# Optimization experiments

Hardware: AMD Instinct MI355X
Metric: run time of the kernel (lower is better)

Reference implementation:

```python
import math
import jax, jax.numpy as jnp
import numpy as np

B, T, E, NH = 2, 4096, 768, 12
HS = E // NH

def setup_inputs() -> dict:
    key = jax.random.key(0)
    k1, k2, k3 = jax.random.split(key, 3)
    x = jax.random.normal(k1, (B, T, E), dtype=jnp.float32)
    W_attn = jax.random.normal(k2, (E, 3 * E), dtype=jnp.float32) * (1.0 / math.sqrt(E))
    b_attn = jnp.zeros((3 * E,), dtype=jnp.float32)
    W_proj = jax.random.normal(k3, (E, E), dtype=jnp.float32) * (1.0 / math.sqrt(E))
    b_proj = jnp.zeros((E,), dtype=jnp.float32)
    return {"x": x, "W_attn": W_attn, "b_attn": b_attn, "W_proj": W_proj, "b_proj": b_proj}

def reference(x, W_attn, b_attn, W_proj, b_proj):
    b, t, e = x.shape
    nh, hs = NH, e // NH
    # QKV projection; split order matches einops '(a nh hs)' with a=3 outermost
    qkv = x @ W_attn + b_attn                      # [b, t, 3e]
    qkv = qkv.reshape(b, t, 3, nh, hs)
    q, k, v = jnp.moveaxis(qkv, 2, 0)              # each [b, t, nh, hs]
    q = jnp.transpose(q, (0, 2, 1, 3))             # [b, nh, t, hs]
    k = jnp.transpose(k, (0, 2, 1, 3))
    v = jnp.transpose(v, (0, 2, 1, 3))
    attn = jnp.einsum('bnth,bnsh->bnts', q, k) * (1.0 / math.sqrt(hs))  # [b, nh, t, t]
    causal = jnp.tril(jnp.ones((t, t), dtype=bool))
    attn = jnp.where(causal[None, None], attn, jnp.float32(-jnp.inf))
    attn = jax.nn.softmax(attn, axis=-1)
    y = jnp.einsum('bnts,bnsh->bnth', attn, v)     # [b, nh, t, hs]
    y = jnp.transpose(y, (0, 2, 1, 3)).reshape(b, t, e)
    return y @ W_proj + b_proj
```

## Files before the change

### kernel.cpp

```cpp
#include <hip/hip_runtime.h>
#include <hip/hip_bf16.h>
#include <cmath>

#define B_   2
#define T_   4096
#define E_   768
#define NH_  12
#define HS_  64
#define QKV_ROW (3 * E_)
#define LSE_N (B_ * NH_ * T_)
#define BTE   (B_ * T_ * E_)

typedef __attribute__((ext_vector_type(8))) short bf16x8;
typedef __attribute__((ext_vector_type(4))) float f32x4;

__device__ __forceinline__ unsigned short f2bf(float f) {
    __hip_bfloat16 h = __float2bfloat16(f);
    return __builtin_bit_cast(unsigned short, h);
}
__device__ __forceinline__ float bf2f(unsigned short s) {
    unsigned int u = (unsigned int)s << 16;
    return __builtin_bit_cast(float, u);
}

#define GLOAD16(gptr, lptr)                                             \
    __builtin_amdgcn_global_load_lds(                                   \
        (const __attribute__((address_space(1))) void*)(gptr),          \
        (__attribute__((address_space(3))) void*)(lptr), 16, 0, 0)

__global__ __launch_bounds__(256) void cvt_x_kernel(
    const float* __restrict__ x, unsigned short* __restrict__ xb)
{
    const int i = (blockIdx.x * 256 + threadIdx.x) * 8;
    const float4 v0 = *(const float4*)&x[i];
    const float4 v1 = *(const float4*)&x[i + 4];
    unsigned short o[8];
    o[0] = f2bf(v0.x); o[1] = f2bf(v0.y); o[2] = f2bf(v0.z); o[3] = f2bf(v0.w);
    o[4] = f2bf(v1.x); o[5] = f2bf(v1.y); o[6] = f2bf(v1.z); o[7] = f2bf(v1.w);
    *(int4*)&xb[i] = *(const int4*)o;
}

__global__ __launch_bounds__(256) void transpose_w_kernel(
    const float* __restrict__ W, unsigned short* __restrict__ Wt, int K, int N)
{
    __shared__ float tile[64][65];
    const int k0  = blockIdx.y * 64;
    const int n0  = blockIdx.x * 64;
    const int tid = threadIdx.x;
    const int tc  = tid & 15;
    const int tr  = tid >> 4;
#pragma unroll
    for (int i = 0; i < 4; ++i) {
        const int k = tr + i * 16;
        const float4 v = *(const float4*)&W[(size_t)(k0 + k) * N + n0 + tc * 4];
        tile[k][tc * 4 + 0] = v.x; tile[k][tc * 4 + 1] = v.y;
        tile[k][tc * 4 + 2] = v.z; tile[k][tc * 4 + 3] = v.w;
    }
    __syncthreads();
    const int nr = tid >> 2;
    const int kc = (tid & 3) * 16;
    unsigned short o[16];
#pragma unroll
    for (int j = 0; j < 16; ++j) o[j] = f2bf(tile[kc + j][nr]);
    unsigned short* dst = &Wt[(size_t)(n0 + nr) * K + k0 + kc];
    *(int4*)dst       = *(const int4*)&o[0];
    *(int4*)(dst + 8) = *(const int4*)&o[8];
}

template<bool OUT_BF16, bool QSCALE>
__global__ __launch_bounds__(256) void gemm_bt_kernel(
    const unsigned short* __restrict__ A,
    const unsigned short* __restrict__ Bt,
    const float* __restrict__ bias, void* __restrict__ Cout,
    int M, int N, int K, int lda)
{
    __shared__ __align__(16) unsigned short Als[128 * 64];
    __shared__ __align__(16) unsigned short Bls[128 * 64];

    const int tid  = threadIdx.x;
    const int m0   = blockIdx.y * 128;
    const int n0   = blockIdx.x * 128;
    const int w    = tid >> 6;
    const int lane = tid & 63;
    const int lr   = lane & 15;
    const int lk   = lane >> 4;
    const int wm   = (w >> 1) * 64;
    const int wn   = (w & 1) * 64;

    f32x4 acc[4][4];
#pragma unroll
    for (int i = 0; i < 4; ++i)
#pragma unroll
        for (int j = 0; j < 4; ++j) acc[i][j] = (f32x4){0.f, 0.f, 0.f, 0.f};

    for (int k0 = 0; k0 < K; k0 += 64) {
        __syncthreads();
#pragma unroll
        for (int c = 0; c < 4; ++c) {
            const int idx = c * 256 + tid;
            const int row = idx >> 3;
            const int g   = (tid & 7) ^ (row & 7);
            GLOAD16(&A[(size_t)(m0 + row) * lda + k0 + g * 8], &Als[idx * 8]);
        }
#pragma unroll
        for (int c = 0; c < 4; ++c) {
            const int idx = c * 256 + tid;
            const int row = idx >> 3;
            const int g   = (tid & 7) ^ (row & 7);
            GLOAD16(&Bt[(size_t)(n0 + row) * K + k0 + g * 8], &Bls[idx * 8]);
        }
        __syncthreads();

#pragma unroll
        for (int kk = 0; kk < 2; ++kk) {
            bf16x8 a[4], b[4];
            const int gp = ((kk * 4 + lk) ^ (lr & 7)) << 3;
#pragma unroll
            for (int i = 0; i < 4; ++i) {
                a[i] = *(const bf16x8*)&Als[(wm + i * 16 + lr) * 64 + gp];
                b[i] = *(const bf16x8*)&Bls[(wn + i * 16 + lr) * 64 + gp];
            }
#pragma unroll
            for (int i = 0; i < 4; ++i)
#pragma unroll
                for (int j = 0; j < 4; ++j)
                    acc[i][j] = __builtin_amdgcn_mfma_f32_16x16x32_bf16(
                        b[j], a[i], acc[i][j], 0, 0, 0);
        }
    }

    const float beta = 0.18033688011f;
#pragma unroll
    for (int i = 0; i < 4; ++i) {
        const int row = m0 + wm + i * 16 + lr;
#pragma unroll
        for (int j = 0; j < 4; ++j) {
            const int nbase = n0 + wn + j * 16 + lk * 4;
            const float4 bv = *(const float4*)&bias[nbase];
            float v0 = acc[i][j][0] + bv.x;
            float v1 = acc[i][j][1] + bv.y;
            float v2 = acc[i][j][2] + bv.z;
            float v3 = acc[i][j][3] + bv.w;
            if (QSCALE && nbase < E_) {
                v0 *= beta; v1 *= beta; v2 *= beta; v3 *= beta;
            }
            if (OUT_BF16) {
                ushort4 o;
                o.x = f2bf(v0); o.y = f2bf(v1); o.z = f2bf(v2); o.w = f2bf(v3);
                *(ushort4*)&((unsigned short*)Cout)[(size_t)row * N + nbase] = o;
            } else {
                float4 o; o.x = v0; o.y = v1; o.z = v2; o.w = v3;
                *(float4*)&((float*)Cout)[(size_t)row * N + nbase] = o;
            }
        }
    }
}

__global__ __launch_bounds__(256) void flash_kernel(
    const unsigned short* __restrict__ qkv,
    unsigned short* __restrict__ y_part,
    float* __restrict__ lsum)
{
    __shared__ __align__(16) unsigned short K_lds[64][72];
    __shared__ __align__(16) unsigned short Vt[64][72];

    const int tid  = threadIdx.x;
    const int w    = tid >> 6;
    const int lane = tid & 63;
    const int lr   = lane & 15;
    const int lk   = lane >> 4;

    const int bid  = blockIdx.x;
    const int xcd  = bid & 7;
    const int rr   = bid >> 3;
    const int g    = (rr >> 5) * 8 + xcd;
    const int head = g >> 1;
    const int z    = g & 1;
    const int qb_lo = rr & 31;
    const int b    = head / NH_;
    const int nh   = head % NH_;
    const int qb_hi = 63 - qb_lo;
    const int q0_lo = qb_lo * 64;
    const int q0_hi = qb_hi * 64;

    const unsigned short* qkv_b = qkv + (size_t)b * T_ * QKV_ROW;

    bf16x8 qf_lo[2], qf_hi[2];
    {
        const unsigned short* qrl =
            qkv_b + (size_t)(q0_lo + w * 16 + lr) * QKV_ROW + nh * HS_;
        qf_lo[0] = *(const bf16x8*)(qrl + lk * 8);
        qf_lo[1] = *(const bf16x8*)(qrl + 32 + lk * 8);
        const unsigned short* qrh =
            qkv_b + (size_t)(q0_hi + w * 16 + lr) * QKV_ROW + nh * HS_;
        qf_hi[0] = *(const bf16x8*)(qrh + lk * 8);
        qf_hi[1] = *(const bf16x8*)(qrh + 32 + lk * 8);
    }

    bf16x8 af1;
    {
        const short one = (lr == 0) ? (short)0x3F80 : (short)0;
#pragma unroll
        for (int j = 0; j < 8; ++j) af1[j] = one;
    }

    f32x4 acc_lo[4], acc_hi[4];
    f32x4 accl_lo = (f32x4){0.f, 0.f, 0.f, 0.f};
    f32x4 accl_hi = (f32x4){0.f, 0.f, 0.f, 0.f};
#pragma unroll
    for (int i = 0; i < 4; ++i) {
        acc_lo[i] = (f32x4){0.f, 0.f, 0.f, 0.f};
        acc_hi[i] = (f32x4){0.f, 0.f, 0.f, 0.f};
    }

    const int sr = tid >> 2;
    const int sc = (tid & 3) * 16;

    auto softmax_pack = [&](f32x4* st, int q0, int kv0, bool diag,
                            bf16x8& pf0, bf16x8& pf1) {
        const int tq = q0 + w * 16 + lr;
        if (diag) {
#pragma unroll
            for (int cb = 0; cb < 4; ++cb)
#pragma unroll
                for (int r = 0; r < 4; ++r) {
                    const int tk = kv0 + cb * 16 + lk * 4 + r;
                    if (tk > tq) st[cb][r] = -INFINITY;
                }
        }
#pragma unroll
        for (int r = 0; r < 4; ++r) {
            pf0[r]     = (short)f2bf(exp2f(st[0][r]));
            pf0[r + 4] = (short)f2bf(exp2f(st[1][r]));
            pf1[r]     = (short)f2bf(exp2f(st[2][r]));
            pf1[r + 4] = (short)f2bf(exp2f(st[3][r]));
        }
    };

    int4 k01r, k23r, v01r, v23r;
    auto load_regs = [&](int j) {
        const unsigned short* krow =
            qkv_b + (size_t)(j * 64 + sr) * QKV_ROW + E_ + nh * HS_ + sc;
        const unsigned short* vrow = krow + E_;
        k01r = *(const int4*)krow;
        k23r = *(const int4*)(krow + 8);
        v01r = *(const int4*)vrow;
        v23r = *(const int4*)(vrow + 8);
    };

    load_regs(z);
    for (int j = z; j <= qb_hi; ) {
        const int kv0 = j * 64;
        const bool do_lo = (j <= qb_lo);
        __syncthreads();
        {
            *(int4*)&K_lds[sr][sc]     = k01r;
            *(int4*)&K_lds[sr][sc + 8] = k23r;
            const unsigned short* vs0 = (const unsigned short*)&v01r;
            const unsigned short* vs1 = (const unsigned short*)&v23r;
            const int kvhi = sr >> 3, kvlo = sr & 7;
#pragma unroll
            for (int i = 0; i < 8; ++i) {
                const int h = sc + i;
                Vt[h][((kvhi ^ (h >> 3)) << 3) + kvlo] = vs0[i];
            }
#pragma unroll
            for (int i = 0; i < 8; ++i) {
                const int h = sc + 8 + i;
                Vt[h][((kvhi ^ (h >> 3)) << 3) + kvlo] = vs1[i];
            }
        }
        __syncthreads();

        const int jn = j + 2;
        if (jn <= qb_hi) load_regs(jn);

        bf16x8 kf[4][2];
#pragma unroll
        for (int cb = 0; cb < 4; ++cb)
#pragma unroll
            for (int ks = 0; ks < 2; ++ks)
                kf[cb][ks] = *(const bf16x8*)&K_lds[cb * 16 + lr][ks * 32 + lk * 8];

        bf16x8 vf[4][2];
#pragma unroll
        for (int cb2 = 0; cb2 < 4; ++cb2) {
            const int row = cb2 * 16 + lr;
            const int sw  = row >> 3;
#pragma unroll
            for (int ks = 0; ks < 2; ++ks) {
                const int cA = ((4 * ks + (lk >> 1)) ^ sw);
                const int cB = ((4 * ks + 2 + (lk >> 1)) ^ sw);
                const int off = 4 * (lk & 1);
                ushort4 a = *(const ushort4*)&Vt[row][cA * 8 + off];
                ushort4 bq = *(const ushort4*)&Vt[row][cB * 8 + off];
                bf16x8 v;
                v[0] = (short)a.x;  v[1] = (short)a.y;
                v[2] = (short)a.z;  v[3] = (short)a.w;
                v[4] = (short)bq.x; v[5] = (short)bq.y;
                v[6] = (short)bq.z; v[7] = (short)bq.w;
                vf[cb2][ks] = v;
            }
        }

        f32x4 st_hi[4], st_lo[4];
        __builtin_amdgcn_s_setprio(1);
#pragma unroll
        for (int cb = 0; cb < 4; ++cb) {
            st_hi[cb] = (f32x4){0.f, 0.f, 0.f, 0.f};
            st_hi[cb] = __builtin_amdgcn_mfma_f32_16x16x32_bf16(kf[cb][0], qf_hi[0], st_hi[cb], 0, 0, 0);
            st_hi[cb] = __builtin_amdgcn_mfma_f32_16x16x32_bf16(kf[cb][1], qf_hi[1], st_hi[cb], 0, 0, 0);
        }
        if (do_lo) {
#pragma unroll
            for (int cb = 0; cb < 4; ++cb) {
                st_lo[cb] = (f32x4){0.f, 0.f, 0.f, 0.f};
                st_lo[cb] = __builtin_amdgcn_mfma_f32_16x16x32_bf16(kf[cb][0], qf_lo[0], st_lo[cb], 0, 0, 0);
                st_lo[cb] = __builtin_amdgcn_mfma_f32_16x16x32_bf16(kf[cb][1], qf_lo[1], st_lo[cb], 0, 0, 0);
            }
        }
        __builtin_amdgcn_s_setprio(0);

        bf16x8 pf0, pf1;
        softmax_pack(st_hi, q0_hi, kv0, j == qb_hi, pf0, pf1);
        __builtin_amdgcn_s_setprio(1);
#pragma unroll
        for (int cb2 = 0; cb2 < 4; ++cb2) {
            acc_hi[cb2] = __builtin_amdgcn_mfma_f32_16x16x32_bf16(vf[cb2][0], pf0, acc_hi[cb2], 0, 0, 0);
            acc_hi[cb2] = __builtin_amdgcn_mfma_f32_16x16x32_bf16(vf[cb2][1], pf1, acc_hi[cb2], 0, 0, 0);
        }
        accl_hi = __builtin_amdgcn_mfma_f32_16x16x32_bf16(af1, pf0, accl_hi, 0, 0, 0);
        accl_hi = __builtin_amdgcn_mfma_f32_16x16x32_bf16(af1, pf1, accl_hi, 0, 0, 0);
        __builtin_amdgcn_s_setprio(0);

        if (do_lo) {
            softmax_pack(st_lo, q0_lo, kv0, j == qb_lo, pf0, pf1);
            __builtin_amdgcn_s_setprio(1);
#pragma unroll
            for (int cb2 = 0; cb2 < 4; ++cb2) {
                acc_lo[cb2] = __builtin_amdgcn_mfma_f32_16x16x32_bf16(vf[cb2][0], pf0, acc_lo[cb2], 0, 0, 0);
                acc_lo[cb2] = __builtin_amdgcn_mfma_f32_16x16x32_bf16(vf[cb2][1], pf1, acc_lo[cb2], 0, 0, 0);
            }
            accl_lo = __builtin_amdgcn_mfma_f32_16x16x32_bf16(af1, pf0, accl_lo, 0, 0, 0);
            accl_lo = __builtin_amdgcn_mfma_f32_16x16x32_bf16(af1, pf1, accl_lo, 0, 0, 0);
            __builtin_amdgcn_s_setprio(0);
        }
        j = jn;
    }

    {
        const float lh = __shfl(accl_hi[0], lr);
        const float ll = __shfl(accl_lo[0], lr);
        unsigned short* yp = y_part + (size_t)z * BTE;
        const float li_hi = (lh > 0.f) ? 1.0f / lh : 0.f;
        const float li_lo = (ll > 0.f) ? 1.0f / ll : 0.f;
        const int tq_hi = q0_hi + w * 16 + lr;
        const int tq_lo = q0_lo + w * 16 + lr;
        unsigned short* yh = &yp[(size_t)(b * T_ + tq_hi) * E_ + nh * HS_];
        unsigned short* yl = &yp[(size_t)(b * T_ + tq_lo) * E_ + nh * HS_];
#pragma unroll
        for (int cb2 = 0; cb2 < 4; ++cb2) {
            ushort4 oh, ol;
            oh.x = f2bf(acc_hi[cb2][0] * li_hi); oh.y = f2bf(acc_hi[cb2][1] * li_hi);
            oh.z = f2bf(acc_hi[cb2][2] * li_hi); oh.w = f2bf(acc_hi[cb2][3] * li_hi);
            ol.x = f2bf(acc_lo[cb2][0] * li_lo); ol.y = f2bf(acc_lo[cb2][1] * li_lo);
            ol.z = f2bf(acc_lo[cb2][2] * li_lo); ol.w = f2bf(acc_lo[cb2][3] * li_lo);
            *(ushort4*)&yh[cb2 * 16 + lk * 4] = oh;
            *(ushort4*)&yl[cb2 * 16 + lk * 4] = ol;
        }
        if (lk == 0) {
            float* lz = lsum + (size_t)z * LSE_N + (size_t)head * T_;
            lz[tq_hi] = lh;
            lz[tq_lo] = ll;
        }
    }
}

__global__ __launch_bounds__(256) void merge_kernel(
    const unsigned short* __restrict__ y_part,
    const float* __restrict__ lsum,
    unsigned short* __restrict__ qkv)
{
    const int i  = blockIdx.x * 256 + threadIdx.x;
    const int e0 = i * 8;
    const int row = e0 / E_;
    const int e   = e0 - row * E_;
    const int nh  = e >> 6;
    const int lidx = ((row >> 12) * NH_ + nh) * T_ + (row & (T_ - 1));
    const float l0 = lsum[lidx];
    const float l1 = lsum[LSE_N + lidx];
    const float inv = 1.0f / (l0 + l1);
    const float w0 = l0 * inv, w1 = l1 * inv;
    bf16x8 p0 = *(const bf16x8*)&y_part[e0];
    bf16x8 p1 = *(const bf16x8*)&y_part[(size_t)BTE + e0];
    ushort4 oa, ob;
    unsigned short o[8];
#pragma unroll
    for (int jj = 0; jj < 8; ++jj)
        o[jj] = f2bf(w0 * bf2f((unsigned short)p0[jj]) +
                     w1 * bf2f((unsigned short)p1[jj]));
    oa.x = o[0]; oa.y = o[1]; oa.z = o[2]; oa.w = o[3];
    ob.x = o[4]; ob.y = o[5]; ob.z = o[6]; ob.w = o[7];
    unsigned short* dst = &qkv[(size_t)row * QKV_ROW + e];
    *(ushort4*)dst = oa;
    *(ushort4*)(dst + 4) = ob;
}

extern "C" void kernel_launch(void* const* d_in, const int* in_sizes, int n_in,
                              void* d_out, int out_size, void* d_ws, size_t ws_size,
                              hipStream_t stream)
{
    const float* x      = (const float*)d_in[0];
    const float* W_attn = (const float*)d_in[1];
    const float* b_attn = (const float*)d_in[2];
    const float* W_proj = (const float*)d_in[3];
    const float* b_proj = (const float*)d_in[4];
    float* out = (float*)d_out;

    char* ws = (char*)d_ws;
    unsigned short* qkv_ws  = (unsigned short*)ws;
    float*          lsum_ws = (float*)(ws + 37748736);
    unsigned short* x_bf16  = (unsigned short*)(ws + 38535168);
    unsigned short* wt_attn = (unsigned short*)(ws + 51118080);
    unsigned short* wt_proj = (unsigned short*)(ws + 54657024);
    unsigned short* y_part  = (unsigned short*)d_out;

    dim3 blk(256);

    cvt_x_kernel<<<dim3(BTE / 8 / 256), blk, 0, stream>>>(x, x_bf16);
    transpose_w_kernel<<<dim3(QKV_ROW / 64, E_ / 64), blk, 0, stream>>>(W_attn, wt_attn, E_, QKV_ROW);
    transpose_w_kernel<<<dim3(E_ / 64, E_ / 64), blk, 0, stream>>>(W_proj, wt_proj, E_, E_);

    gemm_bt_kernel<true, true><<<dim3(QKV_ROW / 128, (B_ * T_) / 128), blk, 0, stream>>>(
        x_bf16, wt_attn, b_attn, (void*)qkv_ws, B_ * T_, QKV_ROW, E_, E_);

    flash_kernel<<<dim3((T_ / 128) * B_ * NH_ * 2), blk, 0, stream>>>(qkv_ws, y_part, lsum_ws);

    merge_kernel<<<dim3(BTE / 8 / 256), blk, 0, stream>>>(y_part, lsum_ws, qkv_ws);

    gemm_bt_kernel<false, false><<<dim3(E_ / 128, (B_ * T_) / 128), blk, 0, stream>>>(
        qkv_ws, wt_proj, b_proj, (void*)out, B_ * T_, E_, E_, QKV_ROW);
}
```

Baseline: 212.7 us.

## Fuse split-attention merge into projection GEMM and merge prep kernels

The three preprocessing launches (x conversion and two weight transposes) become one kernel that dispatches on block index. The separate merge kernel is folded into a new projection GEMM that reads both partial attention outputs and their softmax sums, combines them in registers and writes the merged A tile to LDS. This removes one launch and a full write-then-read of the merged activation. The fused path needs a larger workspace; when that is not available, the code falls back to the old merge-then-GEMM sequence with a compact y buffer.

```diff
diff --git a/kernel.cpp b/kernel.cpp
--- a/kernel.cpp
+++ b/kernel.cpp
@@ -28,27 +28,36 @@
         (const __attribute__((address_space(1))) void*)(gptr),          \
         (__attribute__((address_space(3))) void*)(lptr), 16, 0, 0)
 
-__global__ __launch_bounds__(256) void cvt_x_kernel(
-    const float* __restrict__ x, unsigned short* __restrict__ xb)
-{
-    const int i = (blockIdx.x * 256 + threadIdx.x) * 8;
-    const float4 v0 = *(const float4*)&x[i];
-    const float4 v1 = *(const float4*)&x[i + 4];
-    unsigned short o[8];
-    o[0] = f2bf(v0.x); o[1] = f2bf(v0.y); o[2] = f2bf(v0.z); o[3] = f2bf(v0.w);
-    o[4] = f2bf(v1.x); o[5] = f2bf(v1.y); o[6] = f2bf(v1.z); o[7] = f2bf(v1.w);
-    *(int4*)&xb[i] = *(const int4*)o;
-}
-
-__global__ __launch_bounds__(256) void transpose_w_kernel(
-    const float* __restrict__ W, unsigned short* __restrict__ Wt, int K, int N)
+__global__ __launch_bounds__(256) void prep_kernel(
+    const float* __restrict__ x, unsigned short* __restrict__ xb,
+    const float* __restrict__ Wa, unsigned short* __restrict__ Wat,
+    const float* __restrict__ Wp, unsigned short* __restrict__ Wpt)
 {
     __shared__ float tile[64][65];
-    const int k0  = blockIdx.y * 64;
-    const int n0  = blockIdx.x * 64;
+    const int bid = blockIdx.x;
     const int tid = threadIdx.x;
-    const int tc  = tid & 15;
-    const int tr  = tid >> 4;
+    if (bid < 3072) {
+        const int i = (bid * 256 + tid) * 8;
+        const float4 v0 = *(const float4*)&x[i];
+        const float4 v1 = *(const float4*)&x[i + 4];
+        unsigned short o[8];
+        o[0] = f2bf(v0.x); o[1] = f2bf(v0.y); o[2] = f2bf(v0.z); o[3] = f2bf(v0.w);
+        o[4] = f2bf(v1.x); o[5] = f2bf(v1.y); o[6] = f2bf(v1.z); o[7] = f2bf(v1.w);
+        *(int4*)&xb[i] = *(const int4*)o;
+        return;
+    }
+    const float* W; unsigned short* Wt; int K, N, n0, k0;
+    if (bid < 3504) {
+        const int b2 = bid - 3072;
+        W = Wa; Wt = Wat; K = E_; N = QKV_ROW;
+        n0 = (b2 % 36) * 64; k0 = (b2 / 36) * 64;
+    } else {
+        const int b3 = bid - 3504;
+        W = Wp; Wt = Wpt; K = E_; N = E_;
+        n0 = (b3 % 12) * 64; k0 = (b3 / 12) * 64;
+    }
+    const int tc = tid & 15;
+    const int tr = tid >> 4;
 #pragma unroll
     for (int i = 0; i < 4; ++i) {
         const int k = tr + i * 16;
@@ -152,6 +161,110 @@
                 float4 o; o.x = v0; o.y = v1; o.z = v2; o.w = v3;
                 *(float4*)&((float*)Cout)[(size_t)row * N + nbase] = o;
             }
+        }
+    }
+}
+
+__global__ __launch_bounds__(256) void gemm_proj_fused_kernel(
+    const unsigned short* __restrict__ y_part,
+    const float* __restrict__ lsum,
+    const unsigned short* __restrict__ Bt,
+    const float* __restrict__ bias, float* __restrict__ out)
+{
+    __shared__ __align__(16) unsigned short Als[128 * 64];
+    __shared__ __align__(16) unsigned short Bls[128 * 64];
+
+    const int tid  = threadIdx.x;
+    const int m0   = blockIdx.y * 128;
+    const int n0   = blockIdx.x * 128;
+    const int w    = tid >> 6;
+    const int lane = tid & 63;
+    const int lr   = lane & 15;
+    const int lk   = lane >> 4;
+    const int wm   = (w >> 1) * 64;
+    const int wn   = (w & 1) * 64;
+
+    f32x4 acc[4][4];
+#pragma unroll
+    for (int i = 0; i < 4; ++i)
+#pragma unroll
+        for (int j = 0; j < 4; ++j) acc[i][j] = (f32x4){0.f, 0.f, 0.f, 0.f};
+
+    int4 p0r[4], p1r[4];
+    float l0r[4], l1r[4];
+    auto load_merge = [&](int k0) {
+#pragma unroll
+        for (int c = 0; c < 4; ++c) {
+            const int idx = c * 256 + tid;
+            const int row = idx >> 3;
+            const int g   = (tid & 7) ^ (row & 7);
+            const int m   = m0 + row;
+            const size_t off = (size_t)m * E_ + k0 + g * 8;
+            p0r[c] = *(const int4*)&y_part[off];
+            p1r[c] = *(const int4*)&y_part[(size_t)BTE + off];
+            const int lidx = ((m >> 12) * NH_ + (k0 >> 6)) * T_ + (m & (T_ - 1));
+            l0r[c] = lsum[lidx];
+            l1r[c] = lsum[LSE_N + lidx];
+        }
+    };
+
+    load_merge(0);
+    for (int k0 = 0; k0 < E_; k0 += 64) {
+        __syncthreads();
+#pragma unroll
+        for (int c = 0; c < 4; ++c) {
+            const int idx = c * 256 + tid;
+            const float inv = 1.0f / (l0r[c] + l1r[c]);
+            const float w0 = l0r[c] * inv, w1 = l1r[c] * inv;
+            const unsigned short* a0 = (const unsigned short*)&p0r[c];
+            const unsigned short* a1 = (const unsigned short*)&p1r[c];
+            unsigned short o[8];
+#pragma unroll
+            for (int i = 0; i < 8; ++i)
+                o[i] = f2bf(w0 * bf2f(a0[i]) + w1 * bf2f(a1[i]));
+            *(int4*)&Als[idx * 8] = *(const int4*)o;
+        }
+#pragma unroll
+        for (int c = 0; c < 4; ++c) {
+            const int idx = c * 256 + tid;
+            const int row = idx >> 3;
+            const int g   = (tid & 7) ^ (row & 7);
+            GLOAD16(&Bt[(size_t)(n0 + row) * E_ + k0 + g * 8], &Bls[idx * 8]);
+        }
+        __syncthreads();
+        if (k0 + 64 < E_) load_merge(k0 + 64);
+
+#pragma unroll
+        for (int kk = 0; kk < 2; ++kk) {
+            bf16x8 a[4], b[4];
+            const int gp = ((kk * 4 + lk) ^ (lr & 7)) << 3;
+#pragma unroll
+            for (int i = 0; i < 4; ++i) {
+                a[i] = *(const bf16x8*)&Als[(wm + i * 16 + lr) * 64 + gp];
+                b[i] = *(const bf16x8*)&Bls[(wn + i * 16 + lr) * 64 + gp];
+            }
+#pragma unroll
+            for (int i = 0; i < 4; ++i)
+#pragma unroll
+                for (int j = 0; j < 4; ++j)
+                    acc[i][j] = __builtin_amdgcn_mfma_f32_16x16x32_bf16(
+                        b[j], a[i], acc[i][j], 0, 0, 0);
+        }
+    }
+
+#pragma unroll
+    for (int i = 0; i < 4; ++i) {
+        const int row = m0 + wm + i * 16 + lr;
+#pragma unroll
+        for (int j = 0; j < 4; ++j) {
+            const int nbase = n0 + wn + j * 16 + lk * 4;
+            const float4 bv = *(const float4*)&bias[nbase];
+            float4 o;
+            o.x = acc[i][j][0] + bv.x;
+            o.y = acc[i][j][1] + bv.y;
+            o.z = acc[i][j][2] + bv.z;
+            o.w = acc[i][j][3] + bv.w;
+            *(float4*)&out[(size_t)row * E_ + nbase] = o;
         }
     }
 }
@@ -379,7 +492,7 @@
 __global__ __launch_bounds__(256) void merge_kernel(
     const unsigned short* __restrict__ y_part,
     const float* __restrict__ lsum,
-    unsigned short* __restrict__ qkv)
+    unsigned short* __restrict__ y)
 {
     const int i  = blockIdx.x * 256 + threadIdx.x;
     const int e0 = i * 8;
@@ -401,7 +514,7 @@
                      w1 * bf2f((unsigned short)p1[jj]));
     oa.x = o[0]; oa.y = o[1]; oa.z = o[2]; oa.w = o[3];
     ob.x = o[4]; ob.y = o[5]; ob.z = o[6]; ob.w = o[7];
-    unsigned short* dst = &qkv[(size_t)row * QKV_ROW + e];
+    unsigned short* dst = &y[e0];
     *(ushort4*)dst = oa;
     *(ushort4*)(dst + 4) = ob;
 }
@@ -423,21 +536,30 @@
     unsigned short* x_bf16  = (unsigned short*)(ws + 38535168);
     unsigned short* wt_attn = (unsigned short*)(ws + 51118080);
     unsigned short* wt_proj = (unsigned short*)(ws + 54657024);
-    unsigned short* y_part  = (unsigned short*)d_out;
+    const size_t ypart_off = 55836672;
+    const bool fused = (ws_size >= ypart_off + 2 * (size_t)BTE * 2);
 
     dim3 blk(256);
 
-    cvt_x_kernel<<<dim3(BTE / 8 / 256), blk, 0, stream>>>(x, x_bf16);
-    transpose_w_kernel<<<dim3(QKV_ROW / 64, E_ / 64), blk, 0, stream>>>(W_attn, wt_attn, E_, QKV_ROW);
-    transpose_w_kernel<<<dim3(E_ / 64, E_ / 64), blk, 0, stream>>>(W_proj, wt_proj, E_, E_);
+    prep_kernel<<<dim3(3072 + 432 + 144), blk, 0, stream>>>(
+        x, x_bf16, W_attn, wt_attn, W_proj, wt_proj);
 
     gemm_bt_kernel<true, true><<<dim3(QKV_ROW / 128, (B_ * T_) / 128), blk, 0, stream>>>(
         x_bf16, wt_attn, b_attn, (void*)qkv_ws, B_ * T_, QKV_ROW, E_, E_);
 
-    flash_kernel<<<dim3((T_ / 128) * B_ * NH_ * 2), blk, 0, stream>>>(qkv_ws, y_part, lsum_ws);
-
-    merge_kernel<<<dim3(BTE / 8 / 256), blk, 0, stream>>>(y_part, lsum_ws, qkv_ws);
-
-    gemm_bt_kernel<false, false><<<dim3(E_ / 128, (B_ * T_) / 128), blk, 0, stream>>>(
-        qkv_ws, wt_proj, b_proj, (void*)out, B_ * T_, E_, E_, QKV_ROW);
-}
+    if (fused) {
+        unsigned short* y_part = (unsigned short*)(ws + ypart_off);
+        flash_kernel<<<dim3((T_ / 128) * B_ * NH_ * 2), blk, 0, stream>>>(
+            qkv_ws, y_part, lsum_ws);
+        gemm_proj_fused_kernel<<<dim3(E_ / 128, (B_ * T_) / 128), blk, 0, stream>>>(
+            y_part, lsum_ws, wt_proj, b_proj, out);
+    } else {
+        unsigned short* y_part   = (unsigned short*)d_out;
+        unsigned short* y_merged = x_bf16;
+        flash_kernel<<<dim3((T_ / 128) * B_ * NH_ * 2), blk, 0, stream>>>(
+            qkv_ws, y_part, lsum_ws);
+        merge_kernel<<<dim3(BTE / 8 / 256), blk, 0, stream>>>(y_part, lsum_ws, y_merged);
+        gemm_bt_kernel<false, false><<<dim3(E_ / 128, (B_ * T_) / 128), blk, 0, stream>>>(
+            y_merged, wt_proj, b_proj, (void*)out, B_ * T_, E_, E_, E_);
+    }
+}
```

Result: no change. 214.3 us (+0.7%).
